# Kernel optimization log

Measured on AMD Instinct MI355X. Metric: run time of the kernel, lower is better.

## Reference

```python
import jax, jax.numpy as jnp
import numpy as np

MAX_LEN = 3

def _attention(h, enc, w1, b1, w2):
    # h: [B,H], enc: [B,S,H]
    B, S, H = enc.shape
    hs = jnp.broadcast_to(h[:, None, :], (B, S, H))
    x = jnp.tanh(jnp.concatenate([enc, hs], axis=-1) @ w1.T + b1)  # [B,S,H]
    e = (x @ w2.T)[..., 0]                                         # [B,S]
    alpha = jax.nn.softmax(e, axis=1)
    return jnp.einsum('bs,bsd->bd', alpha, enc)                    # [B,H]

def _gru_cell(x, h, w_ih, w_hh, b_ih, b_hh):
    # torch GRU gate order: r, z, n
    H = h.shape[-1]
    gi = x @ w_ih.T + b_ih   # [B,3H]
    gh = h @ w_hh.T + b_hh
    i_r, i_z, i_n = gi[:, :H], gi[:, H:2*H], gi[:, 2*H:]
    h_r, h_z, h_n = gh[:, :H], gh[:, H:2*H], gh[:, 2*H:]
    r = jax.nn.sigmoid(i_r + h_r)
    z = jax.nn.sigmoid(i_z + h_z)
    n = jnp.tanh(i_n + r * h_n)
    return (1.0 - z) * n + z * h

def setup_inputs() -> dict:
    key = jax.random.key(0)
    ks = jax.random.split(key, 16)
    B, S, H, DW = 1024, 40, 1024, 512
    V0 = V1 = 4000
    EMB_N = V0 + V1 + 1
    sc = lambda fan: 1.0 / np.sqrt(fan)
    inp = {
        'encoder_outputs': jax.random.normal(ks[0], (B, S, H), jnp.float32),
        'encoder_hidden': jax.random.normal(ks[1], (1, B, H), jnp.float32),
        'targets': jax.random.randint(ks[2], (MAX_LEN, B), 0, V0),
        'emb': jax.random.normal(ks[3], (EMB_N, DW), jnp.float32) * 0.02,
        'attn_w1': jax.random.normal(ks[4], (H, 2 * H), jnp.float32) * sc(2 * H),
        'attn_b1': jnp.zeros((H,), jnp.float32),
        'attn_w2': jax.random.normal(ks[5], (1, H), jnp.float32) * sc(H),
        'w_ih': jax.random.normal(ks[6], (3 * H, H + DW), jnp.float32) * sc(H),
        'w_hh': jax.random.normal(ks[7], (3 * H, H), jnp.float32) * sc(H),
        'b_ih': jnp.zeros((3 * H,), jnp.float32),
        'b_hh': jnp.zeros((3 * H,), jnp.float32),
        'out0_w': jax.random.normal(ks[8], (V0, H), jnp.float32) * sc(H),
        'out0_b': jnp.zeros((V0,), jnp.float32),
        'out1_w': jax.random.normal(ks[9], (V1, H), jnp.float32) * sc(H),
        'out1_b': jnp.zeros((V1,), jnp.float32),
    }
    return inp

def reference(encoder_outputs, encoder_hidden, targets, emb, attn_w1, attn_b1,
              attn_w2, w_ih, w_hh, b_ih, b_hh, out0_w, out0_b, out1_w, out1_b):
    B = encoder_outputs.shape[0]
    h = encoder_hidden[0]  # n_layers=1, unidirectional -> init state passthrough
    logs = []
    for t in range(MAX_LEN):
        context = _attention(h, encoder_outputs, attn_w1, attn_b1, attn_w2)
        if t == 0:
            it = jnp.zeros((B,), jnp.int32)
        elif t == 1:
            it = targets[0] + 1
        else:
            it = targets[t - 1] + 36
        x = jnp.concatenate([emb[it], context], axis=1)  # [B, DW+H]
        h = _gru_cell(x, h, w_ih, w_hh, b_ih, b_hh)
        if t == 0 or t == 2:
            logits = h @ out0_w.T + out0_b
        else:
            logits = h @ out1_w.T + out1_b
        logs.append(jax.nn.log_softmax(logits, axis=1))
    return jnp.stack(logs)  # [MAX_LEN, B, V]
```

## Files before the change

kernel.cpp:

```cpp
#include <hip/hip_runtime.h>
#include <hip/hip_bf16.h>
#include <math.h>

#define B_SZ 1024
#define S_SZ 40
#define H_SZ 1024
#define DW_SZ 512
#define V_SZ 4000
#define XW (DW_SZ + H_SZ)
#define NG (4 * H_SZ)

typedef __bf16 bf16x8 __attribute__((ext_vector_type(8)));
typedef float f32x4 __attribute__((ext_vector_type(4)));

__device__ __forceinline__ float fast_tanh(float x) {
    return 1.0f - 2.0f / (1.0f + __expf(2.0f * x));
}
__device__ __forceinline__ float fast_sigmoid(float x) {
    return 1.0f / (1.0f + __expf(-x));
}
__device__ __forceinline__ float bfraw2f(unsigned short u) {
    return __uint_as_float(((unsigned)u) << 16);
}

#define GLL16(gp, lp)                                                                \
    __builtin_amdgcn_global_load_lds((const __attribute__((address_space(1))) void*)(gp), \
                                     (__attribute__((address_space(3))) void*)(lp), 16, 0, 0)

__global__ __launch_bounds__(256, 2) void gemm_bt_pipe128(
    const __hip_bfloat16* __restrict__ A, int lda,
    const __hip_bfloat16* __restrict__ W, int ldw,
    __hip_bfloat16* __restrict__ C, int ldc,
    int nbx, int K) {
    extern __shared__ char smem[];
    const int tid = threadIdx.x;
    const int lane = tid & 63;
    const int wave = tid >> 6;
    const int wm = wave >> 1, wn = wave & 1;
    const int fr = lane & 15, fq = lane >> 4;

    int bid = blockIdx.x;
    { const int cpx = gridDim.x >> 3; bid = (bid & 7) * cpx + (bid >> 3); }
    const int by = bid / nbx;
    const int bm = by * 128;
    const int bn = (bid - by * nbx) * 256;

    const int r0 = tid >> 2;
    const int s0 = (tid & 3) ^ ((tid >> 3) & 3);
    const __hip_bfloat16* gA0 = A + (size_t)(bm + r0) * lda + s0 * 8;
    const __hip_bfloat16* gA1 = A + (size_t)(bm + r0 + 64) * lda + s0 * 8;
    const __hip_bfloat16* gW0 = W + (size_t)(bn + r0) * ldw + s0 * 8;
    const __hip_bfloat16* gW1 = W + (size_t)(bn + r0 + 64) * ldw + s0 * 8;
    const __hip_bfloat16* gW2 = W + (size_t)(bn + r0 + 128) * ldw + s0 * 8;
    const __hip_bfloat16* gW3 = W + (size_t)(bn + r0 + 192) * ldw + s0 * 8;
    const int dst0 = tid * 16;

    int aoff[4], boff[8];
#pragma unroll
    for (int mi = 0; mi < 4; ++mi) {
        const int row = wm * 64 + mi * 16 + fr;
        aoff[mi] = row * 64 + ((fq ^ ((row >> 1) & 3)) << 4);
    }
#pragma unroll
    for (int ni = 0; ni < 8; ++ni) {
        const int col = wn * 128 + ni * 16 + fr;
        boff[ni] = 8192 + col * 64 + ((fq ^ ((col >> 1) & 3)) << 4);
    }

    const int NT = K >> 5;
    f32x4 acc[4][8] = {};

#define STAGE_T(t)                                                    \
    do {                                                              \
        char* sb = smem + ((t) % 3) * 24576;                          \
        const int kk = (t) << 5;                                      \
        GLL16(gA0 + kk, sb + dst0);                                   \
        GLL16(gA1 + kk, sb + dst0 + 4096);                            \
        GLL16(gW0 + kk, sb + 8192 + dst0);                            \
        GLL16(gW1 + kk, sb + 8192 + dst0 + 4096);                     \
        GLL16(gW2 + kk, sb + 8192 + dst0 + 8192);                     \
        GLL16(gW3 + kk, sb + 8192 + dst0 + 12288);                    \
    } while (0)

    STAGE_T(0);
    STAGE_T(1);
    __builtin_amdgcn_sched_barrier(0);
    asm volatile("s_waitcnt vmcnt(6)" ::: "memory");
    __builtin_amdgcn_s_barrier();
    __builtin_amdgcn_sched_barrier(0);

    for (int t = 0; t < NT; ++t) {
        const char* sb = smem + (t % 3) * 24576;
        bf16x8 af[4], bg[8];
#pragma unroll
        for (int ni = 0; ni < 8; ++ni) bg[ni] = *reinterpret_cast<const bf16x8*>(sb + boff[ni]);
#pragma unroll
        for (int mi = 0; mi < 4; ++mi) af[mi] = *reinterpret_cast<const bf16x8*>(sb + aoff[mi]);

        if (t + 2 < NT) STAGE_T(t + 2);

        __builtin_amdgcn_s_setprio(1);
#pragma unroll
        for (int mi = 0; mi < 4; ++mi)
#pragma unroll
            for (int ni = 0; ni < 8; ++ni)
                acc[mi][ni] = __builtin_amdgcn_mfma_f32_16x16x32_bf16(af[mi], bg[ni], acc[mi][ni], 0, 0, 0);
        __builtin_amdgcn_s_setprio(0);

        if (t != NT - 1) {
            __builtin_amdgcn_sched_barrier(0);
            if (t + 2 < NT) asm volatile("s_waitcnt vmcnt(6)" ::: "memory");
            else            asm volatile("s_waitcnt vmcnt(0)" ::: "memory");
            __builtin_amdgcn_s_barrier();
            __builtin_amdgcn_sched_barrier(0);
        }
    }
#undef STAGE_T

#pragma unroll
    for (int mi = 0; mi < 4; ++mi) {
        const int row0 = bm + wm * 64 + mi * 16 + fq * 4;
#pragma unroll
        for (int ni = 0; ni < 8; ++ni) {
            const int col = bn + wn * 128 + ni * 16 + fr;
#pragma unroll
            for (int r = 0; r < 4; ++r)
                C[(size_t)(row0 + r) * ldc + col] = __float2bfloat16(acc[mi][ni][r]);
        }
    }
}

template <int OB, int SWZ>
__global__ __launch_bounds__(256) void gemm_bt_mfma(
    const __hip_bfloat16* __restrict__ A, int lda,
    const __hip_bfloat16* __restrict__ W, int ldw,
    const float* __restrict__ bias,
    void* __restrict__ Cv, int ldc,
    int nbx, int N, int K) {
    __shared__ __align__(16) __hip_bfloat16 As[128 * 32];
    __shared__ __align__(16) __hip_bfloat16 Ws[128 * 32];
    const int tid = threadIdx.x;
    const int lane = tid & 63;
    const int wave = tid >> 6;

    int bid = blockIdx.x;
    if (SWZ) {
        const int cpx = gridDim.x >> 3;
        bid = (bid & 7) * cpx + (bid >> 3);
    }
    const int by = bid / nbx;
    const int bx = bid - by * nbx;
    const int bm = by * 128;
    const int bn = bx * 128;

    const int r0 = tid >> 2;
    const int kk = (tid & 3) * 8;
    const __hip_bfloat16* gA0 = A + (size_t)(bm + r0) * lda + kk;
    const __hip_bfloat16* gA1 = gA0 + (size_t)64 * lda;
    int wrow0 = bn + r0;      if (wrow0 > N - 1) wrow0 = N - 1;
    int wrow1 = bn + r0 + 64; if (wrow1 > N - 1) wrow1 = N - 1;
    const __hip_bfloat16* gW0 = W + (size_t)wrow0 * ldw + kk;
    const __hip_bfloat16* gW1 = W + (size_t)wrow1 * ldw + kk;
    char* As_c = (char*)As + tid * 16;
    char* Ws_c = (char*)Ws + tid * 16;

    const int wr = wave >> 1, wc = wave & 1;
    const int fr = lane & 15, fq = lane >> 4;
    const __hip_bfloat16* Ard = &As[(wr * 64 + fr) * 32 + fq * 8];
    const __hip_bfloat16* Wrd = &Ws[(wc * 64 + fr) * 32 + fq * 8];

    f32x4 acc[4][4] = {};

    for (int k0 = 0; k0 < K; k0 += 32) {
        __syncthreads();
        GLL16(gA0 + k0, As_c);
        GLL16(gA1 + k0, As_c + 4096);
        GLL16(gW0 + k0, Ws_c);
        GLL16(gW1 + k0, Ws_c + 4096);
        __syncthreads();

        bf16x8 af[4], bg[4];
#pragma unroll
        for (int i = 0; i < 4; ++i) {
            af[i] = *reinterpret_cast<const bf16x8*>(Ard + i * 16 * 32);
            bg[i] = *reinterpret_cast<const bf16x8*>(Wrd + i * 16 * 32);
        }
#pragma unroll
        for (int mi = 0; mi < 4; ++mi)
#pragma unroll
            for (int ni = 0; ni < 4; ++ni)
                acc[mi][ni] = __builtin_amdgcn_mfma_f32_16x16x32_bf16(af[mi], bg[ni], acc[mi][ni], 0, 0, 0);
    }

#pragma unroll
    for (int ni = 0; ni < 4; ++ni) {
        const int col = bn + wc * 64 + ni * 16 + fr;
        if (col >= N) continue;
        const float bb = bias ? bias[col] : 0.0f;
#pragma unroll
        for (int mi = 0; mi < 4; ++mi) {
            const int row0 = bm + wr * 64 + mi * 16 + fq * 4;
#pragma unroll
            for (int r = 0; r < 4; ++r) {
                const float v = acc[mi][ni][r] + bb;
                if (OB)
                    reinterpret_cast<__hip_bfloat16*>(Cv)[(size_t)(row0 + r) * ldc + col] = __float2bfloat16(v);
                else
                    reinterpret_cast<float*>(Cv)[(size_t)(row0 + r) * ldc + col] = v;
            }
        }
    }
}

__global__ __launch_bounds__(256) void gemm_dual_mfma(
    const __hip_bfloat16* __restrict__ A,
    const __hip_bfloat16* __restrict__ Wg,
    const __hip_bfloat16* __restrict__ Wo,
    const float* __restrict__ bias_cat,
    const float* __restrict__ ob,
    __hip_bfloat16* __restrict__ hg,
    __hip_bfloat16* __restrict__ lg,
    int full) {
    const int nbx = 64;
    const int bid = blockIdx.x;
    const int by = bid / nbx;
    const int bx = bid - by * nbx;
    const int bm = by * 128;
    const int bn = bx * 128;
    const int is_hg = (bn < NG);
    if (!full && is_hg) return;

    __shared__ __align__(16) __hip_bfloat16 As[128 * 32];
    __shared__ __align__(16) __hip_bfloat16 Ws[128 * 32];
    const int tid = threadIdx.x;
    const int lane = tid & 63;
    const int wave = tid >> 6;

    const __hip_bfloat16* Wb = is_hg ? Wg : Wo;
    const int coff = is_hg ? bn : bn - NG;
    const int nn = is_hg ? NG : V_SZ;

    const int r0 = tid >> 2;
    const int kk = (tid & 3) * 8;
    const __hip_bfloat16* gA0 = A + (size_t)(bm + r0) * H_SZ + kk;
    const __hip_bfloat16* gA1 = gA0 + (size_t)64 * H_SZ;
    int wrow0 = coff + r0;      if (wrow0 > nn - 1) wrow0 = nn - 1;
    int wrow1 = coff + r0 + 64; if (wrow1 > nn - 1) wrow1 = nn - 1;
    const __hip_bfloat16* gW0 = Wb + (size_t)wrow0 * H_SZ + kk;
    const __hip_bfloat16* gW1 = Wb + (size_t)wrow1 * H_SZ + kk;
    char* As_c = (char*)As + tid * 16;
    char* Ws_c = (char*)Ws + tid * 16;

    const int wr = wave >> 1, wc = wave & 1;
    const int fr = lane & 15, fq = lane >> 4;
    const __hip_bfloat16* Ard = &As[(wr * 64 + fr) * 32 + fq * 8];
    const __hip_bfloat16* Wrd = &Ws[(wc * 64 + fr) * 32 + fq * 8];

    f32x4 acc[4][4] = {};

    for (int k0 = 0; k0 < H_SZ; k0 += 32) {
        __syncthreads();
        GLL16(gA0 + k0, As_c);
        GLL16(gA1 + k0, As_c + 4096);
        GLL16(gW0 + k0, Ws_c);
        GLL16(gW1 + k0, Ws_c + 4096);
        __syncthreads();

        bf16x8 af[4], bg[4];
#pragma unroll
        for (int i = 0; i < 4; ++i) {
            af[i] = *reinterpret_cast<const bf16x8*>(Ard + i * 16 * 32);
            bg[i] = *reinterpret_cast<const bf16x8*>(Wrd + i * 16 * 32);
        }
#pragma unroll
        for (int mi = 0; mi < 4; ++mi)
#pragma unroll
            for (int ni = 0; ni < 4; ++ni)
                acc[mi][ni] = __builtin_amdgcn_mfma_f32_16x16x32_bf16(af[mi], bg[ni], acc[mi][ni], 0, 0, 0);
    }

#pragma unroll
    for (int ni = 0; ni < 4; ++ni) {
        const int cl = coff + wc * 64 + ni * 16 + fr;
        if (cl >= nn) continue;
        const float bb = is_hg ? bias_cat[cl] : ob[cl];
#pragma unroll
        for (int mi = 0; mi < 4; ++mi) {
            const int row0 = bm + wr * 64 + mi * 16 + fq * 4;
#pragma unroll
            for (int r = 0; r < 4; ++r) {
                const float v = acc[mi][ni][r] + bb;
                if (is_hg)
                    hg[(size_t)(row0 + r) * NG + cl] = __float2bfloat16(v);
                else
                    lg[(size_t)(row0 + r) * V_SZ + cl] = __float2bfloat16(v);
            }
        }
    }
}

struct CastSeg { const float* src; long long sstride; int c4n; __hip_bfloat16* dst; long long n4; };
__global__ __launch_bounds__(256) void cast_all_kernel(CastSeg s0, CastSeg s1, CastSeg s2,
                                                       CastSeg s3, CastSeg s4, CastSeg s5, CastSeg s6) {
    const long long e0 = s0.n4, e1 = e0 + s1.n4, e2 = e1 + s2.n4,
                    e3 = e2 + s3.n4, e4 = e3 + s4.n4, e5 = e4 + s5.n4, e6 = e5 + s6.n4;
    for (long long i = (long long)blockIdx.x * 256 + threadIdx.x; i < e6;
         i += (long long)gridDim.x * 256) {
        CastSeg sg; long long li = i;
        if (i < e0) { sg = s0; }
        else if (i < e1) { sg = s1; li -= e0; }
        else if (i < e2) { sg = s2; li -= e1; }
        else if (i < e3) { sg = s3; li -= e2; }
        else if (i < e4) { sg = s4; li -= e3; }
        else if (i < e5) { sg = s5; li -= e4; }
        else { sg = s6; li -= e5; }
        const long long r = li / sg.c4n;
        const int c = (int)(li - r * sg.c4n) << 2;
        const float4 v = *reinterpret_cast<const float4*>(sg.src + r * sg.sstride + c);
        union { ushort4 u; __hip_bfloat16 h[4]; } o;
        o.h[0] = __float2bfloat16(v.x); o.h[1] = __float2bfloat16(v.y);
        o.h[2] = __float2bfloat16(v.z); o.h[3] = __float2bfloat16(v.w);
        *reinterpret_cast<ushort4*>(sg.dst + r * (long long)(sg.c4n << 2) + c) = o.u;
    }
}

__global__ __launch_bounds__(256) void small_prep_kernel(
    const float* __restrict__ emb, const int* __restrict__ targets,
    __hip_bfloat16* __restrict__ x0, __hip_bfloat16* __restrict__ x1, __hip_bfloat16* __restrict__ x2,
    const float* __restrict__ enc_h, float* __restrict__ h, __hip_bfloat16* __restrict__ h_bf,
    const float* __restrict__ b1, const float* __restrict__ b_hh, float* __restrict__ bias_cat) {
    const int blk = blockIdx.x;
    const int tid = threadIdx.x;
    if (blk < 3072) {
        if (tid >= 128) return;
        const int t = blk >> 10;
        const int b = blk & 1023;
        int it; __hip_bfloat16* x;
        if (t == 0) { it = 0; x = x0; }
        else if (t == 1) { it = targets[b] + 1; x = x1; }
        else { it = targets[B_SZ + b] + 36; x = x2; }
        float4 v = reinterpret_cast<const float4*>(emb + (size_t)it * DW_SZ)[tid];
        union { ushort4 u; __hip_bfloat16 hh[4]; } o;
        o.hh[0] = __float2bfloat16(v.x); o.hh[1] = __float2bfloat16(v.y);
        o.hh[2] = __float2bfloat16(v.z); o.hh[3] = __float2bfloat16(v.w);
        reinterpret_cast<ushort4*>(x + (size_t)b * XW)[tid] = o.u;
    } else if (blk < 4096) {
        const int i = (blk - 3072) * 256 + tid;
        const float4 v = reinterpret_cast<const float4*>(enc_h)[i];
        reinterpret_cast<float4*>(h)[i] = v;
        union { ushort4 u; __hip_bfloat16 hh[4]; } o;
        o.hh[0] = __float2bfloat16(v.x); o.hh[1] = __float2bfloat16(v.y);
        o.hh[2] = __float2bfloat16(v.z); o.hh[3] = __float2bfloat16(v.w);
        reinterpret_cast<ushort4*>(h_bf)[i] = o.u;
    } else {
        for (int j = tid; j < NG; j += 256)
            bias_cat[j] = (j < H_SZ) ? b1[j] : b_hh[j - H_SZ];
    }
}

__global__ __launch_bounds__(256) void attn_ls_kernel(
    const __hip_bfloat16* __restrict__ enc,
    const __hip_bfloat16* __restrict__ enc_proj,
    const __hip_bfloat16* __restrict__ hg,
    const float* __restrict__ w2,
    __hip_bfloat16* __restrict__ x,
    const __hip_bfloat16* __restrict__ lg,
    float* __restrict__ outp,
    int nattn) {
    const int blk = blockIdx.x;
    const int tid = threadIdx.x;
    const int lane = tid & 63, wave = tid >> 6;
    __shared__ float s_e[S_SZ];
    __shared__ float s_red[4];
    __shared__ float s_bc;

    if (blk < nattn) {
        const int b = blk;
        float hp[16], wv[16];
        const unsigned short* hgrow = reinterpret_cast<const unsigned short*>(hg) + (size_t)b * NG;
#pragma unroll
        for (int p = 0; p < 4; ++p) {
            const int base = p * 256 + lane * 4;
            ushort4 hu = *reinterpret_cast<const ushort4*>(hgrow + base);
            float4 wq = *reinterpret_cast<const float4*>(w2 + base);
            hp[p * 4 + 0] = bfraw2f(hu.x); hp[p * 4 + 1] = bfraw2f(hu.y);
            hp[p * 4 + 2] = bfraw2f(hu.z); hp[p * 4 + 3] = bfraw2f(hu.w);
            wv[p * 4 + 0] = wq.x; wv[p * 4 + 1] = wq.y;
            wv[p * 4 + 2] = wq.z; wv[p * 4 + 3] = wq.w;
        }

        const unsigned short* ep0 = reinterpret_cast<const unsigned short*>(enc_proj) + (size_t)b * S_SZ * H_SZ;
#pragma unroll 2
        for (int i = 0; i < 10; ++i) {
            const int s = wave + 4 * i;
            const unsigned short* row = ep0 + (size_t)s * H_SZ;
            float acc = 0.f;
#pragma unroll
            for (int p = 0; p < 4; ++p) {
                ushort4 eu = *reinterpret_cast<const ushort4*>(row + p * 256 + lane * 4);
                acc += fast_tanh(bfraw2f(eu.x) + hp[p * 4 + 0]) * wv[p * 4 + 0]
                     + fast_tanh(bfraw2f(eu.y) + hp[p * 4 + 1]) * wv[p * 4 + 1]
                     + fast_tanh(bfraw2f(eu.z) + hp[p * 4 + 2]) * wv[p * 4 + 2]
                     + fast_tanh(bfraw2f(eu.w) + hp[p * 4 + 3]) * wv[p * 4 + 3];
            }
#pragma unroll
            for (int off = 32; off > 0; off >>= 1) acc += __shfl_down(acc, off);
            if (lane == 0) s_e[s] = acc;
        }
        __syncthreads();

        float m = -1e30f;
        for (int s = 0; s < S_SZ; ++s) m = fmaxf(m, s_e[s]);
        float sum = 0.f;
        for (int s = 0; s < S_SZ; ++s) sum += __expf(s_e[s] - m);
        const float inv = 1.0f / sum;

        const ushort4* enc_b = reinterpret_cast<const ushort4*>(enc + (size_t)b * S_SZ * H_SZ);
        float4 acc = make_float4(0.f, 0.f, 0.f, 0.f);
        for (int s = 0; s < S_SZ; ++s) {
            const float a = __expf(s_e[s] - m) * inv;
            ushort4 ev = enc_b[s * 256 + tid];
            acc.x += a * bfraw2f(ev.x); acc.y += a * bfraw2f(ev.y);
            acc.z += a * bfraw2f(ev.z); acc.w += a * bfraw2f(ev.w);
        }
        union { ushort4 u; __hip_bfloat16 hh[4]; } o;
        o.hh[0] = __float2bfloat16(acc.x); o.hh[1] = __float2bfloat16(acc.y);
        o.hh[2] = __float2bfloat16(acc.z); o.hh[3] = __float2bfloat16(acc.w);
        reinterpret_cast<ushort4*>(x + (size_t)b * XW + DW_SZ)[tid] = o.u;
    } else {
        const int b = blk - nattn;
        const ushort4* row4 = reinterpret_cast<const ushort4*>(
            reinterpret_cast<const unsigned short*>(lg) + (size_t)b * V_SZ);
        float* orow = outp + (size_t)b * V_SZ;

        float m = -1e30f;
        for (int k = tid; k < V_SZ / 4; k += 256) {
            ushort4 u = row4[k];
            m = fmaxf(m, fmaxf(fmaxf(bfraw2f(u.x), bfraw2f(u.y)), fmaxf(bfraw2f(u.z), bfraw2f(u.w))));
        }
#pragma unroll
        for (int off = 32; off > 0; off >>= 1) m = fmaxf(m, __shfl_down(m, off));
        if (lane == 0) s_red[wave] = m;
        __syncthreads();
        if (tid == 0) s_bc = fmaxf(fmaxf(s_red[0], s_red[1]), fmaxf(s_red[2], s_red[3]));
        __syncthreads();
        m = s_bc;

        float sum = 0.f;
        for (int k = tid; k < V_SZ / 4; k += 256) {
            ushort4 u = row4[k];
            sum += expf(bfraw2f(u.x) - m) + expf(bfraw2f(u.y) - m)
                 + expf(bfraw2f(u.z) - m) + expf(bfraw2f(u.w) - m);
        }
#pragma unroll
        for (int off = 32; off > 0; off >>= 1) sum += __shfl_down(sum, off);
        __syncthreads();
        if (lane == 0) s_red[wave] = sum;
        __syncthreads();
        if (tid == 0) s_bc = logf(s_red[0] + s_red[1] + s_red[2] + s_red[3]) + m;
        __syncthreads();
        const float ls = s_bc;

        for (int k = tid; k < V_SZ / 4; k += 256) {
            ushort4 u = row4[k];
            float4 o = make_float4(bfraw2f(u.x) - ls, bfraw2f(u.y) - ls,
                                   bfraw2f(u.z) - ls, bfraw2f(u.w) - ls);
            reinterpret_cast<float4*>(orow)[k] = o;
        }
    }
}

__global__ __launch_bounds__(256) void gru_gate_kernel(
    const __hip_bfloat16* __restrict__ gi,
    const __hip_bfloat16* __restrict__ hg,
    float* __restrict__ h,
    __hip_bfloat16* __restrict__ h_bf) {
    const int idx = blockIdx.x * 256 + threadIdx.x;
    const int b = idx >> 10;
    const int j = idx & 1023;
    const unsigned short* gib = reinterpret_cast<const unsigned short*>(gi) + (size_t)b * 3 * H_SZ;
    const unsigned short* ghb = reinterpret_cast<const unsigned short*>(hg) + (size_t)b * NG + H_SZ;
    const float i_r = bfraw2f(gib[j]), i_z = bfraw2f(gib[H_SZ + j]), i_n = bfraw2f(gib[2 * H_SZ + j]);
    const float h_r = bfraw2f(ghb[j]), h_z = bfraw2f(ghb[H_SZ + j]), h_n = bfraw2f(ghb[2 * H_SZ + j]);
    const float r = fast_sigmoid(i_r + h_r);
    const float z = fast_sigmoid(i_z + h_z);
    const float n = fast_tanh(i_n + r * h_n);
    const float hv = (1.0f - z) * n + z * h[idx];
    h[idx] = hv;
    h_bf[idx] = __float2bfloat16(hv);
}

extern "C" void kernel_launch(void* const* d_in, const int* in_sizes, int n_in,
                              void* d_out, int out_size, void* d_ws, size_t ws_size,
                              hipStream_t stream) {
    const float* enc    = (const float*)d_in[0];
    const float* enc_h  = (const float*)d_in[1];
    const int*   tgt    = (const int*)d_in[2];
    const float* emb    = (const float*)d_in[3];
    const float* w1     = (const float*)d_in[4];
    const float* b1     = (const float*)d_in[5];
    const float* w2     = (const float*)d_in[6];
    const float* w_ih   = (const float*)d_in[7];
    const float* w_hh   = (const float*)d_in[8];
    const float* b_ih   = (const float*)d_in[9];
    const float* b_hh   = (const float*)d_in[10];
    const float* out0_w = (const float*)d_in[11];
    const float* out0_b = (const float*)d_in[12];
    const float* out1_w = (const float*)d_in[13];
    const float* out1_b = (const float*)d_in[14];
    float* out = (float*)d_out;

    char* wp = (char*)d_ws;
    auto carve = [&](size_t bytes) { char* p = wp; wp += (bytes + 255) & ~(size_t)255; return p; };
    __hip_bfloat16* enc_bf  = (__hip_bfloat16*)carve((size_t)B_SZ * S_SZ * H_SZ * 2);
    __hip_bfloat16* encp_bf = (__hip_bfloat16*)carve((size_t)B_SZ * S_SZ * H_SZ * 2);
    __hip_bfloat16* w1a_bf  = (__hip_bfloat16*)carve((size_t)H_SZ * H_SZ * 2);
    __hip_bfloat16* wcat_bf = (__hip_bfloat16*)carve((size_t)NG * H_SZ * 2);
    __hip_bfloat16* wih_bf  = (__hip_bfloat16*)carve((size_t)3 * H_SZ * XW * 2);
    __hip_bfloat16* o0_bf   = (__hip_bfloat16*)carve((size_t)V_SZ * H_SZ * 2);
    __hip_bfloat16* o1_bf   = (__hip_bfloat16*)carve((size_t)V_SZ * H_SZ * 2);
    float*          bias_cat= (float*)carve((size_t)NG * 4);
    float*          h       = (float*)carve((size_t)B_SZ * H_SZ * 4);
    __hip_bfloat16* h_bf    = (__hip_bfloat16*)carve((size_t)B_SZ * H_SZ * 2);
    __hip_bfloat16* hg_bf   = (__hip_bfloat16*)carve((size_t)B_SZ * NG * 2);
    __hip_bfloat16* x_bf[3];
    for (int t = 0; t < 3; ++t) x_bf[t] = (__hip_bfloat16*)carve((size_t)B_SZ * XW * 2);
    __hip_bfloat16* gi_bf   = (__hip_bfloat16*)carve((size_t)B_SZ * 3 * H_SZ * 2);
    __hip_bfloat16* lg_bf   = (__hip_bfloat16*)carve((size_t)B_SZ * V_SZ * 2);

    {
        CastSeg s0{w1,        2 * H_SZ, H_SZ / 4, w1a_bf,                        (long long)H_SZ * H_SZ / 4};
        CastSeg s1{w1 + H_SZ, 2 * H_SZ, H_SZ / 4, wcat_bf,                       (long long)H_SZ * H_SZ / 4};
        CastSeg s2{w_hh,      H_SZ,     H_SZ / 4, wcat_bf + (size_t)H_SZ * H_SZ, (long long)3 * H_SZ * H_SZ / 4};
        CastSeg s3{w_ih,      XW,       XW / 4,   wih_bf,                        (long long)3 * H_SZ * XW / 4};
        CastSeg s4{out0_w,    H_SZ,     H_SZ / 4, o0_bf,                         (long long)V_SZ * H_SZ / 4};
        CastSeg s5{out1_w,    H_SZ,     H_SZ / 4, o1_bf,                         (long long)V_SZ * H_SZ / 4};
        CastSeg s6{enc,       H_SZ,     H_SZ / 4, enc_bf,                        (long long)B_SZ * S_SZ * H_SZ / 4};
        cast_all_kernel<<<4096, 256, 0, stream>>>(s0, s1, s2, s3, s4, s5, s6);
    }
    small_prep_kernel<<<4097, 256, 0, stream>>>(emb, tgt, x_bf[0], x_bf[1], x_bf[2],
                                                enc_h, h, h_bf, b1, b_hh, bias_cat);

    gemm_bt_pipe128<<<(B_SZ * S_SZ / 128) * (H_SZ / 256), 256, 3 * 24576, stream>>>(
        enc_bf, H_SZ, w1a_bf, H_SZ, encp_bf, H_SZ, H_SZ / 256, H_SZ);

    gemm_bt_mfma<1, 0><<<(B_SZ / 128) * (NG / 128), 256, 0, stream>>>(
        h_bf, H_SZ, wcat_bf, H_SZ, bias_cat, hg_bf, NG, NG / 128, NG, H_SZ);

    attn_ls_kernel<<<B_SZ, 256, 0, stream>>>(enc_bf, encp_bf, hg_bf, w2, x_bf[0],
                                             lg_bf, out, B_SZ);

    for (int t = 0; t < 3; ++t) {
        gemm_bt_mfma<1, 0><<<(B_SZ / 128) * (3 * H_SZ / 128), 256, 0, stream>>>(
            x_bf[t], XW, wih_bf, XW, b_ih, gi_bf, 3 * H_SZ, 3 * H_SZ / 128, 3 * H_SZ, XW);

        gru_gate_kernel<<<(B_SZ * H_SZ) / 256, 256, 0, stream>>>(gi_bf, hg_bf, h, h_bf);

        const __hip_bfloat16* ow = (t == 1) ? o1_bf : o0_bf;
        const float* ob = (t == 1) ? out1_b : out0_b;
        gemm_dual_mfma<<<(B_SZ / 128) * 64, 256, 0, stream>>>(
            h_bf, wcat_bf, ow, bias_cat, ob, hg_bf, lg_bf, (t < 2) ? 1 : 0);

        float* outp = out + (size_t)t * B_SZ * V_SZ;
        if (t < 2) {
            attn_ls_kernel<<<2 * B_SZ, 256, 0, stream>>>(enc_bf, encp_bf, hg_bf, w2, x_bf[t + 1],
                                                         lg_bf, outp, B_SZ);
        } else {
            attn_ls_kernel<<<B_SZ, 256, 0, stream>>>(enc_bf, encp_bf, hg_bf, w2, x_bf[0],
                                                     lg_bf, outp, 0);
        }
    }
}
```

Measured before the change: 538.1 us.

## Concatenate gate and output weights into padded matrices and reuse generic GEMM

```diff
diff --git a/kernel.cpp b/kernel.cpp
--- a/kernel.cpp
+++ b/kernel.cpp
@@ -8,7 +8,7 @@
 #define DW_SZ 512
 #define V_SZ 4000
 #define XW (DW_SZ + H_SZ)
-#define NG (4 * H_SZ)
+#define NGL 8192
 
 typedef __bf16 bf16x8 __attribute__((ext_vector_type(8)));
 typedef float f32x4 __attribute__((ext_vector_type(4)));
@@ -21,6 +21,12 @@
 }
 __device__ __forceinline__ float bfraw2f(unsigned short u) {
     return __uint_as_float(((unsigned)u) << 16);
+}
+__device__ __forceinline__ ushort4 cvt4(float4 v) {
+    union { ushort4 u; __hip_bfloat16 h[4]; } o;
+    o.h[0] = __float2bfloat16(v.x); o.h[1] = __float2bfloat16(v.y);
+    o.h[2] = __float2bfloat16(v.z); o.h[3] = __float2bfloat16(v.w);
+    return o.u;
 }
 
 #define GLL16(gp, lp)                                                                \
@@ -212,115 +218,58 @@
     }
 }
 
-__global__ __launch_bounds__(256) void gemm_dual_mfma(
-    const __hip_bfloat16* __restrict__ A,
-    const __hip_bfloat16* __restrict__ Wg,
-    const __hip_bfloat16* __restrict__ Wo,
-    const float* __restrict__ bias_cat,
-    const float* __restrict__ ob,
-    __hip_bfloat16* __restrict__ hg,
-    __hip_bfloat16* __restrict__ lg,
-    int full) {
-    const int nbx = 64;
-    const int bid = blockIdx.x;
-    const int by = bid / nbx;
-    const int bx = bid - by * nbx;
-    const int bm = by * 128;
-    const int bn = bx * 128;
-    const int is_hg = (bn < NG);
-    if (!full && is_hg) return;
-
-    __shared__ __align__(16) __hip_bfloat16 As[128 * 32];
-    __shared__ __align__(16) __hip_bfloat16 Ws[128 * 32];
-    const int tid = threadIdx.x;
-    const int lane = tid & 63;
-    const int wave = tid >> 6;
-
-    const __hip_bfloat16* Wb = is_hg ? Wg : Wo;
-    const int coff = is_hg ? bn : bn - NG;
-    const int nn = is_hg ? NG : V_SZ;
-
-    const int r0 = tid >> 2;
-    const int kk = (tid & 3) * 8;
-    const __hip_bfloat16* gA0 = A + (size_t)(bm + r0) * H_SZ + kk;
-    const __hip_bfloat16* gA1 = gA0 + (size_t)64 * H_SZ;
-    int wrow0 = coff + r0;      if (wrow0 > nn - 1) wrow0 = nn - 1;
-    int wrow1 = coff + r0 + 64; if (wrow1 > nn - 1) wrow1 = nn - 1;
-    const __hip_bfloat16* gW0 = Wb + (size_t)wrow0 * H_SZ + kk;
-    const __hip_bfloat16* gW1 = Wb + (size_t)wrow1 * H_SZ + kk;
-    char* As_c = (char*)As + tid * 16;
-    char* Ws_c = (char*)Ws + tid * 16;
-
-    const int wr = wave >> 1, wc = wave & 1;
-    const int fr = lane & 15, fq = lane >> 4;
-    const __hip_bfloat16* Ard = &As[(wr * 64 + fr) * 32 + fq * 8];
-    const __hip_bfloat16* Wrd = &Ws[(wc * 64 + fr) * 32 + fq * 8];
-
-    f32x4 acc[4][4] = {};
-
-    for (int k0 = 0; k0 < H_SZ; k0 += 32) {
-        __syncthreads();
-        GLL16(gA0 + k0, As_c);
-        GLL16(gA1 + k0, As_c + 4096);
-        GLL16(gW0 + k0, Ws_c);
-        GLL16(gW1 + k0, Ws_c + 4096);
-        __syncthreads();
-
-        bf16x8 af[4], bg[4];
-#pragma unroll
-        for (int i = 0; i < 4; ++i) {
-            af[i] = *reinterpret_cast<const bf16x8*>(Ard + i * 16 * 32);
-            bg[i] = *reinterpret_cast<const bf16x8*>(Wrd + i * 16 * 32);
-        }
-#pragma unroll
-        for (int mi = 0; mi < 4; ++mi)
-#pragma unroll
-            for (int ni = 0; ni < 4; ++ni)
-                acc[mi][ni] = __builtin_amdgcn_mfma_f32_16x16x32_bf16(af[mi], bg[ni], acc[mi][ni], 0, 0, 0);
-    }
-
-#pragma unroll
-    for (int ni = 0; ni < 4; ++ni) {
-        const int cl = coff + wc * 64 + ni * 16 + fr;
-        if (cl >= nn) continue;
-        const float bb = is_hg ? bias_cat[cl] : ob[cl];
-#pragma unroll
-        for (int mi = 0; mi < 4; ++mi) {
-            const int row0 = bm + wr * 64 + mi * 16 + fq * 4;
-#pragma unroll
-            for (int r = 0; r < 4; ++r) {
-                const float v = acc[mi][ni][r] + bb;
-                if (is_hg)
-                    hg[(size_t)(row0 + r) * NG + cl] = __float2bfloat16(v);
-                else
-                    lg[(size_t)(row0 + r) * V_SZ + cl] = __float2bfloat16(v);
-            }
-        }
-    }
-}
-
-struct CastSeg { const float* src; long long sstride; int c4n; __hip_bfloat16* dst; long long n4; };
-__global__ __launch_bounds__(256) void cast_all_kernel(CastSeg s0, CastSeg s1, CastSeg s2,
-                                                       CastSeg s3, CastSeg s4, CastSeg s5, CastSeg s6) {
-    const long long e0 = s0.n4, e1 = e0 + s1.n4, e2 = e1 + s2.n4,
-                    e3 = e2 + s3.n4, e4 = e3 + s4.n4, e5 = e4 + s5.n4, e6 = e5 + s6.n4;
-    for (long long i = (long long)blockIdx.x * 256 + threadIdx.x; i < e6;
-         i += (long long)gridDim.x * 256) {
-        CastSeg sg; long long li = i;
-        if (i < e0) { sg = s0; }
-        else if (i < e1) { sg = s1; li -= e0; }
-        else if (i < e2) { sg = s2; li -= e1; }
-        else if (i < e3) { sg = s3; li -= e2; }
-        else if (i < e4) { sg = s4; li -= e3; }
-        else if (i < e5) { sg = s5; li -= e4; }
-        else { sg = s6; li -= e5; }
-        const long long r = li / sg.c4n;
-        const int c = (int)(li - r * sg.c4n) << 2;
-        const float4 v = *reinterpret_cast<const float4*>(sg.src + r * sg.sstride + c);
-        union { ushort4 u; __hip_bfloat16 h[4]; } o;
-        o.h[0] = __float2bfloat16(v.x); o.h[1] = __float2bfloat16(v.y);
-        o.h[2] = __float2bfloat16(v.z); o.h[3] = __float2bfloat16(v.w);
-        *reinterpret_cast<ushort4*>(sg.dst + r * (long long)(sg.c4n << 2) + c) = o.u;
+#define F4_ENC (B_SZ * S_SZ * H_SZ / 4)
+#define F4_W1A (H_SZ * H_SZ / 4)
+#define F4_W1H (H_SZ * H_SZ / 4)
+#define F4_WHH (3 * H_SZ * H_SZ / 4)
+#define F4_WIH (3 * H_SZ * XW / 4)
+#define F4_O0  (V_SZ * H_SZ / 4)
+#define F4_O1  (V_SZ * H_SZ / 4)
+#define CE0 (F4_ENC)
+#define CE1 (CE0 + F4_W1A)
+#define CE2 (CE1 + F4_W1H)
+#define CE3 (CE2 + F4_WHH)
+#define CE4 (CE3 + F4_WIH)
+#define CE5 (CE4 + F4_O0)
+#define CE6 (CE5 + F4_O1)
+__global__ __launch_bounds__(256) void cast_fast_kernel(
+    const float* __restrict__ enc, const float* __restrict__ w1,
+    const float* __restrict__ whh, const float* __restrict__ wih,
+    const float* __restrict__ o0, const float* __restrict__ o1,
+    __hip_bfloat16* __restrict__ enc_bf, __hip_bfloat16* __restrict__ w1a_bf,
+    __hip_bfloat16* __restrict__ wall0, __hip_bfloat16* __restrict__ wall1,
+    __hip_bfloat16* __restrict__ wih_bf) {
+    const int i = blockIdx.x * 256 + threadIdx.x;
+    ushort4* wall0_u = reinterpret_cast<ushort4*>(wall0);
+    ushort4* wall1_u = reinterpret_cast<ushort4*>(wall1);
+    if (i < CE0) {
+        const float4 v = reinterpret_cast<const float4*>(enc)[i];
+        reinterpret_cast<ushort4*>(enc_bf)[i] = cvt4(v);
+    } else if (i < CE1) {
+        const int li = i - CE0;
+        const int r = li >> 8, c = li & 255;
+        const float4 v = reinterpret_cast<const float4*>(w1)[r * 512 + c];
+        reinterpret_cast<ushort4*>(w1a_bf)[li] = cvt4(v);
+    } else if (i < CE2) {
+        const int li = i - CE1;
+        const int r = li >> 8, c = li & 255;
+        const ushort4 u = cvt4(reinterpret_cast<const float4*>(w1)[r * 512 + 256 + c]);
+        wall0_u[li] = u;
+        wall1_u[li] = u;
+    } else if (i < CE3) {
+        const int li = i - CE2;
+        const ushort4 u = cvt4(reinterpret_cast<const float4*>(whh)[li]);
+        wall0_u[262144 + li] = u;
+        wall1_u[262144 + li] = u;
+    } else if (i < CE4) {
+        const int li = i - CE3;
+        reinterpret_cast<ushort4*>(wih_bf)[li] = cvt4(reinterpret_cast<const float4*>(wih)[li]);
+    } else if (i < CE5) {
+        const int li = i - CE4;
+        wall0_u[1048576 + li] = cvt4(reinterpret_cast<const float4*>(o0)[li]);
+    } else {
+        const int li = i - CE5;
+        wall1_u[1048576 + li] = cvt4(reinterpret_cast<const float4*>(o1)[li]);
     }
 }
 
@@ -328,7 +277,9 @@
     const float* __restrict__ emb, const int* __restrict__ targets,
     __hip_bfloat16* __restrict__ x0, __hip_bfloat16* __restrict__ x1, __hip_bfloat16* __restrict__ x2,
     const float* __restrict__ enc_h, float* __restrict__ h, __hip_bfloat16* __restrict__ h_bf,
-    const float* __restrict__ b1, const float* __restrict__ b_hh, float* __restrict__ bias_cat) {
+    const float* __restrict__ b1, const float* __restrict__ b_hh,
+    const float* __restrict__ o0b, const float* __restrict__ o1b,
+    float* __restrict__ bias0, float* __restrict__ bias1) {
     const int blk = blockIdx.x;
     const int tid = threadIdx.x;
     if (blk < 3072) {
@@ -340,31 +291,32 @@
         else if (t == 1) { it = targets[b] + 1; x = x1; }
         else { it = targets[B_SZ + b] + 36; x = x2; }
         float4 v = reinterpret_cast<const float4*>(emb + (size_t)it * DW_SZ)[tid];
-        union { ushort4 u; __hip_bfloat16 hh[4]; } o;
-        o.hh[0] = __float2bfloat16(v.x); o.hh[1] = __float2bfloat16(v.y);
-        o.hh[2] = __float2bfloat16(v.z); o.hh[3] = __float2bfloat16(v.w);
-        reinterpret_cast<ushort4*>(x + (size_t)b * XW)[tid] = o.u;
+        reinterpret_cast<ushort4*>(x + (size_t)b * XW)[tid] = cvt4(v);
     } else if (blk < 4096) {
         const int i = (blk - 3072) * 256 + tid;
         const float4 v = reinterpret_cast<const float4*>(enc_h)[i];
         reinterpret_cast<float4*>(h)[i] = v;
-        union { ushort4 u; __hip_bfloat16 hh[4]; } o;
-        o.hh[0] = __float2bfloat16(v.x); o.hh[1] = __float2bfloat16(v.y);
-        o.hh[2] = __float2bfloat16(v.z); o.hh[3] = __float2bfloat16(v.w);
-        reinterpret_cast<ushort4*>(h_bf)[i] = o.u;
+        reinterpret_cast<ushort4*>(h_bf)[i] = cvt4(v);
     } else {
-        for (int j = tid; j < NG; j += 256)
-            bias_cat[j] = (j < H_SZ) ? b1[j] : b_hh[j - H_SZ];
+        float* bt = (blk == 4096) ? bias0 : bias1;
+        const float* ob = (blk == 4096) ? o0b : o1b;
+        for (int j = tid; j < NGL; j += 256) {
+            float v;
+            if (j < H_SZ) v = b1[j];
+            else if (j < 4 * H_SZ) v = b_hh[j - H_SZ];
+            else if (j < 4 * H_SZ + V_SZ) v = ob[j - 4 * H_SZ];
+            else v = 0.0f;
+            bt[j] = v;
+        }
     }
 }
 
 __global__ __launch_bounds__(256) void attn_ls_kernel(
     const __hip_bfloat16* __restrict__ enc,
     const __hip_bfloat16* __restrict__ enc_proj,
-    const __hip_bfloat16* __restrict__ hg,
+    const __hip_bfloat16* __restrict__ hgl,
     const float* __restrict__ w2,
     __hip_bfloat16* __restrict__ x,
-    const __hip_bfloat16* __restrict__ lg,
     float* __restrict__ outp,
     int nattn) {
     const int blk = blockIdx.x;
@@ -377,7 +329,7 @@
     if (blk < nattn) {
         const int b = blk;
         float hp[16], wv[16];
-        const unsigned short* hgrow = reinterpret_cast<const unsigned short*>(hg) + (size_t)b * NG;
+        const unsigned short* hgrow = reinterpret_cast<const unsigned short*>(hgl) + (size_t)b * NGL;
 #pragma unroll
         for (int p = 0; p < 4; ++p) {
             const int base = p * 256 + lane * 4;
@@ -423,14 +375,11 @@
             acc.x += a * bfraw2f(ev.x); acc.y += a * bfraw2f(ev.y);
             acc.z += a * bfraw2f(ev.z); acc.w += a * bfraw2f(ev.w);
         }
-        union { ushort4 u; __hip_bfloat16 hh[4]; } o;
-        o.hh[0] = __float2bfloat16(acc.x); o.hh[1] = __float2bfloat16(acc.y);
-        o.hh[2] = __float2bfloat16(acc.z); o.hh[3] = __float2bfloat16(acc.w);
-        reinterpret_cast<ushort4*>(x + (size_t)b * XW + DW_SZ)[tid] = o.u;
+        reinterpret_cast<ushort4*>(x + (size_t)b * XW + DW_SZ)[tid] = cvt4(acc);
     } else {
         const int b = blk - nattn;
         const ushort4* row4 = reinterpret_cast<const ushort4*>(
-            reinterpret_cast<const unsigned short*>(lg) + (size_t)b * V_SZ);
+            reinterpret_cast<const unsigned short*>(hgl) + (size_t)b * NGL + 4096);
         float* orow = outp + (size_t)b * V_SZ;
 
         float m = -1e30f;
@@ -472,14 +421,14 @@
 
 __global__ __launch_bounds__(256) void gru_gate_kernel(
     const __hip_bfloat16* __restrict__ gi,
-    const __hip_bfloat16* __restrict__ hg,
+    const __hip_bfloat16* __restrict__ hgl,
     float* __restrict__ h,
     __hip_bfloat16* __restrict__ h_bf) {
     const int idx = blockIdx.x * 256 + threadIdx.x;
     const int b = idx >> 10;
     const int j = idx & 1023;
     const unsigned short* gib = reinterpret_cast<const unsigned short*>(gi) + (size_t)b * 3 * H_SZ;
-    const unsigned short* ghb = reinterpret_cast<const unsigned short*>(hg) + (size_t)b * NG + H_SZ;
+    const unsigned short* ghb = reinterpret_cast<const unsigned short*>(hgl) + (size_t)b * NGL + H_SZ;
     const float i_r = bfraw2f(gib[j]), i_z = bfraw2f(gib[H_SZ + j]), i_n = bfraw2f(gib[2 * H_SZ + j]);
     const float h_r = bfraw2f(ghb[j]), h_z = bfraw2f(ghb[H_SZ + j]), h_n = bfraw2f(ghb[2 * H_SZ + j]);
     const float r = fast_sigmoid(i_r + h_r);
@@ -515,59 +464,59 @@
     __hip_bfloat16* enc_bf  = (__hip_bfloat16*)carve((size_t)B_SZ * S_SZ * H_SZ * 2);
     __hip_bfloat16* encp_bf = (__hip_bfloat16*)carve((size_t)B_SZ * S_SZ * H_SZ * 2);
     __hip_bfloat16* w1a_bf  = (__hip_bfloat16*)carve((size_t)H_SZ * H_SZ * 2);
-    __hip_bfloat16* wcat_bf = (__hip_bfloat16*)carve((size_t)NG * H_SZ * 2);
+    __hip_bfloat16* wall0   = (__hip_bfloat16*)carve((size_t)NGL * H_SZ * 2);
+    __hip_bfloat16* wall1   = (__hip_bfloat16*)carve((size_t)NGL * H_SZ * 2);
     __hip_bfloat16* wih_bf  = (__hip_bfloat16*)carve((size_t)3 * H_SZ * XW * 2);
-    __hip_bfloat16* o0_bf   = (__hip_bfloat16*)carve((size_t)V_SZ * H_SZ * 2);
-    __hip_bfloat16* o1_bf   = (__hip_bfloat16*)carve((size_t)V_SZ * H_SZ * 2);
-    float*          bias_cat= (float*)carve((size_t)NG * 4);
+    float*          bias0   = (float*)carve((size_t)NGL * 4);
+    float*          bias1   = (float*)carve((size_t)NGL * 4);
     float*          h       = (float*)carve((size_t)B_SZ * H_SZ * 4);
     __hip_bfloat16* h_bf    = (__hip_bfloat16*)carve((size_t)B_SZ * H_SZ * 2);
-    __hip_bfloat16* hg_bf   = (__hip_bfloat16*)carve((size_t)B_SZ * NG * 2);
+    __hip_bfloat16* hgl     = (__hip_bfloat16*)carve((size_t)B_SZ * NGL * 2);
     __hip_bfloat16* x_bf[3];
     for (int t = 0; t < 3; ++t) x_bf[t] = (__hip_bfloat16*)carve((size_t)B_SZ * XW * 2);
     __hip_bfloat16* gi_bf   = (__hip_bfloat16*)carve((size_t)B_SZ * 3 * H_SZ * 2);
-    __hip_bfloat16* lg_bf   = (__hip_bfloat16*)carve((size_t)B_SZ * V_SZ * 2);
-
-    {
-        CastSeg s0{w1,        2 * H_SZ, H_SZ / 4, w1a_bf,                        (long long)H_SZ * H_SZ / 4};
-        CastSeg s1{w1 + H_SZ, 2 * H_SZ, H_SZ / 4, wcat_bf,                       (long long)H_SZ * H_SZ / 4};
-        CastSeg s2{w_hh,      H_SZ,     H_SZ / 4, wcat_bf + (size_t)H_SZ * H_SZ, (long long)3 * H_SZ * H_SZ / 4};
-        CastSeg s3{w_ih,      XW,       XW / 4,   wih_bf,                        (long long)3 * H_SZ * XW / 4};
-        CastSeg s4{out0_w,    H_SZ,     H_SZ / 4, o0_bf,                         (long long)V_SZ * H_SZ / 4};
-        CastSeg s5{out1_w,    H_SZ,     H_SZ / 4, o1_bf,                         (long long)V_SZ * H_SZ / 4};
-        CastSeg s6{enc,       H_SZ,     H_SZ / 4, enc_bf,                        (long long)B_SZ * S_SZ * H_SZ / 4};
-        cast_all_kernel<<<4096, 256, 0, stream>>>(s0, s1, s2, s3, s4, s5, s6);
-    }
-    small_prep_kernel<<<4097, 256, 0, stream>>>(emb, tgt, x_bf[0], x_bf[1], x_bf[2],
-                                                enc_h, h, h_bf, b1, b_hh, bias_cat);
+
+    cast_fast_kernel<<<CE6 / 256, 256, 0, stream>>>(enc, w1, w_hh, w_ih, out0_w, out1_w,
+                                                    enc_bf, w1a_bf, wall0, wall1, wih_bf);
+    hipMemsetAsync(wall0 + (size_t)(4 * H_SZ + V_SZ) * H_SZ, 0, (size_t)96 * H_SZ * 2, stream);
+    hipMemsetAsync(wall1 + (size_t)(4 * H_SZ + V_SZ) * H_SZ, 0, (size_t)96 * H_SZ * 2, stream);
+    small_prep_kernel<<<4098, 256, 0, stream>>>(emb, tgt, x_bf[0], x_bf[1], x_bf[2],
+                                                enc_h, h, h_bf, b1, b_hh, out0_b, out1_b,
+                                                bias0, bias1);
 
     gemm_bt_pipe128<<<(B_SZ * S_SZ / 128) * (H_SZ / 256), 256, 3 * 24576, stream>>>(
         enc_bf, H_SZ, w1a_bf, H_SZ, encp_bf, H_SZ, H_SZ / 256, H_SZ);
 
-    gemm_bt_mfma<1, 0><<<(B_SZ / 128) * (NG / 128), 256, 0, stream>>>(
-        h_bf, H_SZ, wcat_bf, H_SZ, bias_cat, hg_bf, NG, NG / 128, NG, H_SZ);
-
-    attn_ls_kernel<<<B_SZ, 256, 0, stream>>>(enc_bf, encp_bf, hg_bf, w2, x_bf[0],
-                                             lg_bf, out, B_SZ);
+    gemm_bt_mfma<1, 0><<<(B_SZ / 128) * 32, 256, 0, stream>>>(
+        h_bf, H_SZ, wall0, H_SZ, bias0, hgl, NGL, 32, 4 * H_SZ, H_SZ);
+
+    attn_ls_kernel<<<B_SZ, 256, 0, stream>>>(enc_bf, encp_bf, hgl, w2, x_bf[0], out, B_SZ);
 
     for (int t = 0; t < 3; ++t) {
-        gemm_bt_mfma<1, 0><<<(B_SZ / 128) * (3 * H_SZ / 128), 256, 0, stream>>>(
-            x_bf[t], XW, wih_bf, XW, b_ih, gi_bf, 3 * H_SZ, 3 * H_SZ / 128, 3 * H_SZ, XW);
-
-        gru_gate_kernel<<<(B_SZ * H_SZ) / 256, 256, 0, stream>>>(gi_bf, hg_bf, h, h_bf);
-
-        const __hip_bfloat16* ow = (t == 1) ? o1_bf : o0_bf;
-        const float* ob = (t == 1) ? out1_b : out0_b;
-        gemm_dual_mfma<<<(B_SZ / 128) * 64, 256, 0, stream>>>(
-            h_bf, wcat_bf, ow, bias_cat, ob, hg_bf, lg_bf, (t < 2) ? 1 : 0);
+        gemm_bt_mfma<1, 0><<<(B_SZ / 128) * 24, 256, 0, stream>>>(
+            x_bf[t], XW, wih_bf, XW, b_ih, gi_bf, 3 * H_SZ, 24, 3 * H_SZ, XW);
+
+        gru_gate_kernel<<<(B_SZ * H_SZ) / 256, 256, 0, stream>>>(gi_bf, hgl, h, h_bf);
+
+        if (t == 0) {
+            gemm_bt_mfma<1, 0><<<(B_SZ / 128) * 64, 256, 0, stream>>>(
+                h_bf, H_SZ, wall0, H_SZ, bias0, hgl, NGL, 64, NGL, H_SZ);
+        } else if (t == 1) {
+            gemm_bt_mfma<1, 0><<<(B_SZ / 128) * 64, 256, 0, stream>>>(
+                h_bf, H_SZ, wall1, H_SZ, bias1, hgl, NGL, 64, NGL, H_SZ);
+        } else {
+            gemm_bt_mfma<1, 0><<<(B_SZ / 128) * 32, 256, 0, stream>>>(
+                h_bf, H_SZ, wall0 + (size_t)4 * H_SZ * H_SZ, H_SZ, bias0 + 4 * H_SZ,
+                hgl + 4 * H_SZ, NGL, 32, 4 * H_SZ, H_SZ);
+        }
 
         float* outp = out + (size_t)t * B_SZ * V_SZ;
         if (t < 2) {
-            attn_ls_kernel<<<2 * B_SZ, 256, 0, stream>>>(enc_bf, encp_bf, hg_bf, w2, x_bf[t + 1],
-                                                         lg_bf, outp, B_SZ);
+            attn_ls_kernel<<<2 * B_SZ, 256, 0, stream>>>(enc_bf, encp_bf, hgl, w2, x_bf[t + 1],
+                                                         outp, B_SZ);
         } else {
-            attn_ls_kernel<<<B_SZ, 256, 0, stream>>>(enc_bf, encp_bf, hg_bf, w2, x_bf[0],
-                                                     lg_bf, outp, 0);
-        }
-    }
-}
+            attn_ls_kernel<<<B_SZ, 256, 0, stream>>>(enc_bf, encp_bf, hgl, w2, x_bf[0],
+                                                     outp, 0);
+        }
+    }
+}
```

After: 546.0 us. About the same (+1.5%).
